# Performance work log

Hardware: AMD Instinct MI355X
Metric: run time of the kernel (lower is better)

Reference implementation:

```python
import jax, jax.numpy as jnp
import numpy as np

EPS = 1e-5
NEG_SLOPE = 0.2


def _batched_dynamic_conv(x, kernels):
    # x: [B, C, H, W]; kernels: [B, Cout, Cin, 3, 3]. Per-sample distinct
    # kernels == one grouped conv with feature_group_count = B.
    B, C, H, W = x.shape
    Cout = kernels.shape[1]
    xg = x.reshape(1, B * C, H, W)
    kg = kernels.reshape(B * Cout, C, 3, 3)
    y = jax.lax.conv_general_dilated(
        xg, kg, window_strides=(1, 1), padding=((1, 1), (1, 1)),
        feature_group_count=B,
        dimension_numbers=('NCHW', 'OIHW', 'NCHW'))
    return y.reshape(B, Cout, H, W)


def _instance_norm(y):
    # InstanceNorm2d(affine=False): per (b, c) over spatial dims, biased var.
    mean = jnp.mean(y, axis=(2, 3), keepdims=True)
    var = jnp.var(y, axis=(2, 3), keepdims=True)
    return (y - mean) * jax.lax.rsqrt(var + EPS)


def _leaky_relu(y):
    return jnp.where(y >= 0, y, NEG_SLOPE * y)


def setup_inputs() -> dict:
    key = jax.random.key(0)
    k1, k2, k3 = jax.random.split(key, 3)
    B, C, H, W = 16, 64, 128, 128
    x = jax.random.normal(k1, (B, C, H, W), dtype=jnp.float32)
    kernel1 = jax.random.normal(k2, (B, C, C, 3, 3), dtype=jnp.float32) * 0.05
    kernel2 = jax.random.normal(k3, (B, C, C, 3, 3), dtype=jnp.float32) * 0.05
    return {"x": x, "kernel1": kernel1, "kernel2": kernel2}


def reference(x, kernel1, kernel2):
    h = _leaky_relu(_instance_norm(_batched_dynamic_conv(x, kernel1)))
    h = _instance_norm(_batched_dynamic_conv(h, kernel2))
    return _leaky_relu(x + h)
```

## Files before the change

### kernel.cpp

```cpp
#include <hip/hip_runtime.h>
#include <stdint.h>
#include <stddef.h>

#define BATCH 16
#define CH    64
#define IH    128
#define IW    128
#define HW    (IH*IW)

#define PROW 8320
#define PB   1081600
#define SEG  2112

typedef __attribute__((ext_vector_type(8))) short short8;
typedef __attribute__((ext_vector_type(4))) short short4v;
typedef __attribute__((ext_vector_type(4))) float f32x4;
typedef __attribute__((ext_vector_type(2))) float f32x2;

__device__ __forceinline__ float bf2f(short s) {
    union { unsigned int u; float f; } v;
    v.u = ((unsigned int)(unsigned short)s) << 16;
    return v.f;
}
__device__ __forceinline__ short f2bf(float f) {
    union { float f; unsigned int u; } v; v.f = f;
    unsigned int r = v.u + 0x7fffu + ((v.u >> 16) & 1u);
    return (short)(r >> 16);
}

__device__ __forceinline__ void gload_lds16(const short* g, short* l) {
    __builtin_amdgcn_global_load_lds(
        (const __attribute__((address_space(1))) void*)g,
        (__attribute__((address_space(3))) void*)l, 16, 0, 0);
}

__global__ __launch_bounds__(256) void prep_all(const float* __restrict__ x,
                                                const float* __restrict__ w1,
                                                const float* __restrict__ w2,
                                                short* __restrict__ xpad,
                                                short* __restrict__ w1t,
                                                short* __restrict__ w2t) {
    const int bid = blockIdx.x;
    const int t = threadIdx.x;
    if (bid < 2048) {
        __shared__ float tile[CH * 129];
        const int b = bid >> 7;
        const int y = bid & 127;
        const float* src = x + (size_t)b * CH * HW + (size_t)y * IW;
        #pragma unroll
        for (int i = 0; i < 32; ++i) {
            int lin = i * 256 + t;
            int c = lin >> 7, xx = lin & 127;
            tile[c * 129 + xx] = src[(size_t)c * HW + xx];
        }
        __syncthreads();
        unsigned int* dst = (unsigned int*)(xpad) + (size_t)b * (PB / 2) + (size_t)(y + 1) * (PROW / 2);
        #pragma unroll
        for (int j = 0; j < 16; ++j) {
            int lin = j * 256 + t;
            int c2 = lin & 31, xx = lin >> 5;
            unsigned int lo = (unsigned int)(unsigned short)f2bf(tile[(2 * c2) * 129 + xx]);
            unsigned int hi = (unsigned int)(unsigned short)f2bf(tile[(2 * c2 + 1) * 129 + xx]);
            dst[(c2 >> 4) * 2080 + (xx + 1) * 16 + (c2 & 15)] = lo | (hi << 16);
        }
    } else if (bid < 2560) {
        int b2 = bid - 2048;
        const float* src = w1; short* dst = w1t;
        if (b2 >= 256) { src = w2; dst = w2t; b2 -= 256; }
        int gt = b2 * 256 + t;
        int ci   = gt & 31;
        int cout = (gt >> 5) & 63;
        int cc   = (gt >> 11) & 1;
        int b    = gt >> 12;
        const float* s = src + ((size_t)(b * 64 + cout)) * 576 + (cc * 32 + ci) * 9;
        short* d = dst + ((size_t)(b * 2 + cc) * 9) * 2048 + cout * 32 + ci;
        #pragma unroll
        for (int tap = 0; tap < 9; ++tap)
            d[tap * 2048] = f2bf(s[tap]);
    } else {
        int b2 = bid - 2560;
        short* p = xpad + (size_t)b2 * PB;
        const short8 z = {0,0,0,0,0,0,0,0};
        #pragma unroll
        for (int i = 0; i < 17; ++i) {
            int s = i * 256 + t;
            if (s >= 4128) break;
            if (s < 2080) {
                int row = (s < 1040) ? 0 : 129;
                int o = (s < 1040 ? s : s - 1040) * 8;
                *(short8*)&p[(size_t)row * PROW + o] = z;
            } else {
                int u = s - 2080;
                int k = u & 3, col = (u >> 2) & 1, cc = (u >> 3) & 1, pr = (u >> 4) + 1;
                *(short8*)&p[(size_t)pr * PROW + cc * 4160 + (col ? 129 * 32 : 0) + k * 8] = z;
            }
        }
    }
}

template<bool FUSED>
__global__ __launch_bounds__(256, 1) void conv_kernel(
    const short* __restrict__ in, const short* __restrict__ wt,
    short* __restrict__ out, const float* __restrict__ nrm,
    float* __restrict__ part_s, float* __restrict__ part_q) {

    __shared__ short act[2][12 * SEG];

    const int g    = blockIdx.x;
    const int b    = g >> 4;
    const int t    = threadIdx.x;
    const int lane = t & 63;
    const int wave = t >> 6;
    const int l15  = lane & 15;
    const int q    = lane >> 4;

    const short* inB = in + (size_t)b * PB;
    const short* wgl = wt + (size_t)b * 36864;
    const int aoff = l15 * 32 + q * 8;

    const int scc = wave & 1;
    f32x2 sb[8];
    if (FUSED) {
        const int ci0 = (lane & 3) * 8;
        #pragma unroll
        for (int j = 0; j < 8; ++j)
            sb[j] = ((const f32x2*)nrm)[b * CH + scc * 32 + ci0 + j];
    }

    short8 stg[15];


    auto stage_issue = [&](int tt, short* buf) {
        const int xp0 = (tt & 1) * 64;
        const int quad = ((g & 15) << 1) + (tt >> 1);
        #pragma unroll
        for (int k = 0; k < 3; ++k) {
            const int s = wave + k * 4;
            const int rg = quad * 4 + (s >> 1);
            const short* gseg = inB + (size_t)rg * PROW + (s & 1) * 4160 + xp0 * 32;
            short* lseg = buf + s * SEG;
            #pragma unroll
            for (int c = 0; c < 4; ++c)
                gload_lds16(gseg + c * 512 + lane * 8, lseg + c * 512);
            if (lane < 8)
                gload_lds16(gseg + 2048 + lane * 8, lseg + 2048);
        }
    };

    auto stage_load = [&](int tt) {
        const int xp0 = (tt & 1) * 64;
        const int quad = ((g & 15) << 1) + (tt >> 1);
        #pragma unroll
        for (int k = 0; k < 3; ++k) {
            const int s = wave + k * 4;
            const int rg = quad * 4 + (s >> 1);
            const short* gseg = inB + (size_t)rg * PROW + (s & 1) * 4160 + xp0 * 32;
            #pragma unroll
            for (int c = 0; c < 5; ++c) {
                short8 v = {0,0,0,0,0,0,0,0};
                if (c < 4 || lane < 8)
                    v = *(const short8*)&gseg[c * 512 + lane * 8];
                stg[k * 5 + c] = v;
            }
        }
    };

    auto stage_write = [&](int tt, short* buf) {
        const int ph2 = tt & 1;
        const int quad = ((g & 15) << 1) + (tt >> 1);
        #pragma unroll
        for (int k = 0; k < 3; ++k) {
            const int s = wave + k * 4;
            const int rg = quad * 4 + (s >> 1);
            const bool rowpad = (rg == 0) || (rg == 129);
            short* lseg = buf + s * SEG;
            #pragma unroll
            for (int c = 0; c < 5; ++c) {
                if (c < 4 || lane < 8) {
                    short8 v = stg[k * 5 + c];
                    const int lpx = c * 16 + (lane >> 2);
                    const bool xm = (ph2 == 0 && lpx == 0) || (ph2 == 1 && lpx == 65);
                    short8 o;
                    if (rowpad || xm) {
                        o = (short8){0,0,0,0,0,0,0,0};
                    } else {
                        #pragma unroll
                        for (int j = 0; j < 8; ++j) {
                            float f = sb[j].x * bf2f(v[j]) + sb[j].y;
                            f = f >= 0.f ? f : 0.2f * f;
                            o[j] = f2bf(f);
                        }
                    }
                    *(short8*)&lseg[c * 512 + lane * 8] = o;
                }
            }
        }
    };

    short8 a2[2][4];
    #pragma unroll
    for (int mi = 0; mi < 4; ++mi)
        a2[0][mi] = *(const short8*)&wgl[aoff + mi * 512];

    if (FUSED) { stage_load(0); stage_write(0, act[0]); }
    else       stage_issue(0, act[0]);
    __syncthreads();

    #pragma unroll 1
    for (int tt = 0; tt < 4; ++tt) {
        short* bufr = act[tt & 1];
        short* bufw = act[(tt + 1) & 1];

        if (tt < 3) {
            if (FUSED) stage_load(tt + 1);
            else       stage_issue(tt + 1, bufw);
        }

        const int ph2 = tt & 1;
        const int quad = ((g & 15) << 1) + (tt >> 1);
        const int xp0 = ph2 * 64;
        const int y0 = quad * 4 + wave;

        const f32x4 zero4 = {0.f, 0.f, 0.f, 0.f};
        f32x4 acc[4][4];
        #pragma unroll
        for (int mi = 0; mi < 4; ++mi)
            #pragma unroll
            for (int ni = 0; ni < 4; ++ni) acc[mi][ni] = zero4;

        #pragma unroll
        for (int s = 0; s < 18; ++s) {
            const int cc = s / 9, tap = s % 9;
            const int dy = tap / 3, dx = tap % 3;
            const short* anext = wgl + (((s + 1) % 18) * 2048) + aoff;
            #pragma unroll
            for (int mi = 0; mi < 4; ++mi)
                a2[(s + 1) & 1][mi] = *(const short8*)&anext[mi * 512];
            const int segb = ((wave + dy) * 2 + cc) * SEG;
            short8 bb[4];
            #pragma unroll
            for (int ni = 0; ni < 4; ++ni)
                bb[ni] = *(const short8*)&bufr[segb + (dx + ni * 16 + l15) * 32 + q * 8];
            #pragma unroll
            for (int mi = 0; mi < 4; ++mi)
                #pragma unroll
                for (int ni = 0; ni < 4; ++ni)
                    acc[mi][ni] = __builtin_amdgcn_mfma_f32_16x16x32_bf16(
                        a2[s & 1][mi], bb[ni], acc[mi][ni], 0, 0, 0);
        }

        if (FUSED && tt < 3) stage_write(tt + 1, bufw);

        const int pbase = ((b * 128 + y0) * 2 + ph2) * 64;
        #pragma unroll
        for (int mi = 0; mi < 4; ++mi) {
            float psum[4] = {0.f,0.f,0.f,0.f};
            float psq[4]  = {0.f,0.f,0.f,0.f};
            #pragma unroll
            for (int ni = 0; ni < 4; ++ni) {
                int xx = xp0 + ni * 16 + l15;
                size_t base = (size_t)b * PB + (size_t)(1 + y0) * PROW
                              + (mi >> 1) * 4160 + (size_t)(1 + xx) * 32
                              + (mi & 1) * 16 + q * 4;
                short4v o;
                #pragma unroll
                for (int gg = 0; gg < 4; ++gg) {
                    float v = acc[mi][ni][gg];
                    o[gg] = f2bf(v);
                    psum[gg] += v;
                    psq[gg]  += v * v;
                }
                *(short4v*)&out[base] = o;
            }
            #pragma unroll
            for (int gg = 0; gg < 4; ++gg) {
                float s = psum[gg], s2 = psq[gg];
                #pragma unroll
                for (int off = 1; off < 16; off <<= 1) {
                    s  += __shfl_xor(s,  off, 64);
                    s2 += __shfl_xor(s2, off, 64);
                }
                if (l15 == 0) {
                    int idx = pbase + mi * 16 + q * 4 + gg;
                    part_s[idx] = s;
                    part_q[idx] = s2;
                }
            }
        }

        __syncthreads();
    }
}

__global__ __launch_bounds__(256) void finalize_stats(const float* __restrict__ part_s,
                                                      const float* __restrict__ part_q,
                                                      float* __restrict__ nrm) {
    __shared__ float red[2][4][64];
    const int b = blockIdx.x;
    const int c = threadIdx.x & 63;
    const int g = threadIdx.x >> 6;
    const float* ps = part_s + (size_t)b * 16384 + c;
    const float* pq = part_q + (size_t)b * 16384 + c;
    float s = 0.f, s2 = 0.f;
    #pragma unroll 8
    for (int r = 0; r < 64; ++r) {
        s  += ps[(g * 64 + r) * 64];
        s2 += pq[(g * 64 + r) * 64];
    }
    red[0][g][c] = s;
    red[1][g][c] = s2;
    __syncthreads();
    if (threadIdx.x < 64) {
        float S = red[0][0][c] + red[0][1][c] + red[0][2][c] + red[0][3][c];
        float Q = red[1][0][c] + red[1][1][c] + red[1][2][c] + red[1][3][c];
        const float inv = 1.0f / (float)HW;
        float mean = S * inv;
        float var = Q * inv - mean * mean;
        float scale = rsqrtf(var + 1e-5f);
        f32x2 sb = {scale, -mean * scale};
        ((f32x2*)nrm)[b * CH + c] = sb;
    }
}

__global__ __launch_bounds__(256) void final_kernel(const float* __restrict__ x,
                                                    const short* __restrict__ y2,
                                                    const float* __restrict__ nrm,
                                                    float* __restrict__ out) {
    __shared__ float tile[64 * 65];
    const int x0 = blockIdx.x * 64;
    const int y  = blockIdx.y;
    const int b  = blockIdx.z;
    const int t  = threadIdx.x;
    const f32x2* nb = (const f32x2*)nrm + b * CH;
    const size_t rowb = (size_t)b * PB + (size_t)(y + 1) * PROW;
    #pragma unroll
    for (int i = 0; i < 2; ++i) {
        int s = i * 256 + t;
        int xx = s >> 3;
        int c0 = (s & 7) * 8;
        int cc = c0 >> 5, cl = c0 & 31;
        short8 v = *(const short8*)&y2[rowb + cc * 4160 + (size_t)(x0 + xx + 1) * 32 + cl];
        #pragma unroll
        for (int j = 0; j < 8; ++j) {
            f32x2 sb = nb[c0 + j];
            tile[(c0 + j) * 65 + xx] = sb.x * bf2f(v[j]) + sb.y;
        }
    }
    __syncthreads();
    #pragma unroll
    for (int i = 0; i < 4; ++i) {
        int lin = i * 1024 + t * 4;
        int c = lin >> 6;
        int xx = lin & 63;
        size_t g = ((size_t)(b * CH + c) * IH + y) * IW + x0 + xx;
        f32x4 xv = *(const f32x4*)&x[g];
        f32x4 o;
        #pragma unroll
        for (int k = 0; k < 4; ++k) {
            float f = xv[k] + tile[c * 65 + xx + k];
            o[k] = f >= 0.f ? f : 0.2f * f;
        }
        *(f32x4*)&out[g] = o;
    }
}

extern "C" void kernel_launch(void* const* d_in, const int* in_sizes, int n_in,
                              void* d_out, int out_size, void* d_ws, size_t ws_size,
                              hipStream_t stream) {
    const float* x  = (const float*)d_in[0];
    const float* w1 = (const float*)d_in[1];
    const float* w2 = (const float*)d_in[2];
    float* out = (float*)d_out;
    char* ws = (char*)d_ws;

    const size_t SZ_PAD  = 34611200ull;
    const size_t SZ_PART = 1048576ull;
    short* xpad = (short*)(ws);
    short* hpad = (short*)(ws + SZ_PAD);
    short* w1t  = (short*)(ws + 2 * SZ_PAD);
    short* w2t  = (short*)(ws + 2 * SZ_PAD + 1179648ull);
    float* ps1  = (float*)(ws + 2 * SZ_PAD + 2359296ull);
    float* pq1  = (float*)(ws + 2 * SZ_PAD + 2359296ull + SZ_PART);
    float* ps2  = (float*)(ws + 2 * SZ_PAD + 2359296ull + 2 * SZ_PART);
    float* pq2  = (float*)(ws + 2 * SZ_PAD + 2359296ull + 3 * SZ_PART);
    float* nrm1 = (float*)(ws + 2 * SZ_PAD + 2359296ull + 4 * SZ_PART);
    float* nrm2 = nrm1 + BATCH * CH * 2;

    if (ws_size < 2 * SZ_PAD + 2359296ull + 4 * SZ_PART + 8192) return;

    prep_all<<<2576, 256, 0, stream>>>(x, w1, w2, xpad, w1t, w2t);
    conv_kernel<false><<<256, 256, 0, stream>>>(xpad, w1t, hpad, nullptr, ps1, pq1);
    finalize_stats<<<16, 256, 0, stream>>>(ps1, pq1, nrm1);
    conv_kernel<true><<<256, 256, 0, stream>>>(hpad, w2t, xpad, nrm1, ps2, pq2);
    finalize_stats<<<16, 256, 0, stream>>>(ps2, pq2, nrm2);
    final_kernel<<<dim3(2, 128, 16), 256, 0, stream>>>(x, xpad, nrm2, out);
}
```

Measured before the change: 243.3 us.

## Split conv kernel into producer staging waves and MFMA consumer waves

```diff
diff --git a/kernel.cpp b/kernel.cpp
--- a/kernel.cpp
+++ b/kernel.cpp
@@ -99,7 +99,7 @@
 }
 
 template<bool FUSED>
-__global__ __launch_bounds__(256, 1) void conv_kernel(
+__global__ __launch_bounds__(512, 2) void conv_kernel(
     const short* __restrict__ in, const short* __restrict__ wt,
     short* __restrict__ out, const float* __restrict__ nrm,
     float* __restrict__ part_s, float* __restrict__ part_q) {
@@ -118,177 +118,173 @@
     const short* wgl = wt + (size_t)b * 36864;
     const int aoff = l15 * 32 + q * 8;
 
-    const int scc = wave & 1;
-    f32x2 sb[8];
-    if (FUSED) {
-        const int ci0 = (lane & 3) * 8;
-        #pragma unroll
-        for (int j = 0; j < 8; ++j)
-            sb[j] = ((const f32x2*)nrm)[b * CH + scc * 32 + ci0 + j];
-    }
-
-    short8 stg[15];
-
-
-    auto stage_issue = [&](int tt, short* buf) {
-        const int xp0 = (tt & 1) * 64;
-        const int quad = ((g & 15) << 1) + (tt >> 1);
-        #pragma unroll
-        for (int k = 0; k < 3; ++k) {
-            const int s = wave + k * 4;
-            const int rg = quad * 4 + (s >> 1);
-            const short* gseg = inB + (size_t)rg * PROW + (s & 1) * 4160 + xp0 * 32;
-            short* lseg = buf + s * SEG;
+    if (wave >= 4) {
+        const int p = wave - 4;
+        f32x2 sb[8];
+        if (FUSED) {
+            const int scc = p & 1;
+            const int ci0 = (lane & 3) * 8;
             #pragma unroll
-            for (int c = 0; c < 4; ++c)
-                gload_lds16(gseg + c * 512 + lane * 8, lseg + c * 512);
-            if (lane < 8)
-                gload_lds16(gseg + 2048 + lane * 8, lseg + 2048);
-        }
-    };
-
-    auto stage_load = [&](int tt) {
-        const int xp0 = (tt & 1) * 64;
-        const int quad = ((g & 15) << 1) + (tt >> 1);
-        #pragma unroll
-        for (int k = 0; k < 3; ++k) {
-            const int s = wave + k * 4;
-            const int rg = quad * 4 + (s >> 1);
-            const short* gseg = inB + (size_t)rg * PROW + (s & 1) * 4160 + xp0 * 32;
-            #pragma unroll
-            for (int c = 0; c < 5; ++c) {
-                short8 v = {0,0,0,0,0,0,0,0};
-                if (c < 4 || lane < 8)
-                    v = *(const short8*)&gseg[c * 512 + lane * 8];
-                stg[k * 5 + c] = v;
+            for (int j = 0; j < 8; ++j)
+                sb[j] = ((const f32x2*)nrm)[b * CH + scc * 32 + ci0 + j];
+        }
+
+        auto stage = [&](int tt, short* buf) {
+            const int ph2 = tt & 1;
+            const int xp0 = ph2 * 64;
+            const int quad = ((g & 15) << 1) + (tt >> 1);
+            if (!FUSED) {
+                #pragma unroll
+                for (int k = 0; k < 3; ++k) {
+                    const int s = p + k * 4;
+                    const int rg = quad * 4 + (s >> 1);
+                    const short* gseg = inB + (size_t)rg * PROW + (s & 1) * 4160 + xp0 * 32;
+                    short* lseg = buf + s * SEG;
+                    #pragma unroll
+                    for (int c = 0; c < 4; ++c)
+                        gload_lds16(gseg + c * 512 + lane * 8, lseg + c * 512);
+                    if (lane < 8)
+                        gload_lds16(gseg + 2048 + lane * 8, lseg + 2048);
+                }
+            } else {
+                short8 stg[15];
+                #pragma unroll
+                for (int k = 0; k < 3; ++k) {
+                    const int s = p + k * 4;
+                    const int rg = quad * 4 + (s >> 1);
+                    const short* gseg = inB + (size_t)rg * PROW + (s & 1) * 4160 + xp0 * 32;
+                    #pragma unroll
+                    for (int c = 0; c < 5; ++c) {
+                        short8 v = {0,0,0,0,0,0,0,0};
+                        if (c < 4 || lane < 8)
+                            v = *(const short8*)&gseg[c * 512 + lane * 8];
+                        stg[k * 5 + c] = v;
+                    }
+                }
+                #pragma unroll
+                for (int k = 0; k < 3; ++k) {
+                    const int s = p + k * 4;
+                    const int rg = quad * 4 + (s >> 1);
+                    const bool rowpad = (rg == 0) || (rg == 129);
+                    short* lseg = buf + s * SEG;
+                    #pragma unroll
+                    for (int c = 0; c < 5; ++c) {
+                        if (c < 4 || lane < 8) {
+                            short8 v = stg[k * 5 + c];
+                            const int lpx = c * 16 + (lane >> 2);
+                            const bool xm = (ph2 == 0 && lpx == 0) || (ph2 == 1 && lpx == 65);
+                            short8 o;
+                            if (rowpad || xm) {
+                                o = (short8){0,0,0,0,0,0,0,0};
+                            } else {
+                                #pragma unroll
+                                for (int j = 0; j < 8; ++j) {
+                                    float f = sb[j].x * bf2f(v[j]) + sb[j].y;
+                                    f = f >= 0.f ? f : 0.2f * f;
+                                    o[j] = f2bf(f);
+                                }
+                            }
+                            *(short8*)&lseg[c * 512 + lane * 8] = o;
+                        }
+                    }
+                }
             }
-        }
-    };
-
-    auto stage_write = [&](int tt, short* buf) {
-        const int ph2 = tt & 1;
-        const int quad = ((g & 15) << 1) + (tt >> 1);
-        #pragma unroll
-        for (int k = 0; k < 3; ++k) {
-            const int s = wave + k * 4;
-            const int rg = quad * 4 + (s >> 1);
-            const bool rowpad = (rg == 0) || (rg == 129);
-            short* lseg = buf + s * SEG;
-            #pragma unroll
-            for (int c = 0; c < 5; ++c) {
-                if (c < 4 || lane < 8) {
-                    short8 v = stg[k * 5 + c];
-                    const int lpx = c * 16 + (lane >> 2);
-                    const bool xm = (ph2 == 0 && lpx == 0) || (ph2 == 1 && lpx == 65);
-                    short8 o;
-                    if (rowpad || xm) {
-                        o = (short8){0,0,0,0,0,0,0,0};
-                    } else {
-                        #pragma unroll
-                        for (int j = 0; j < 8; ++j) {
-                            float f = sb[j].x * bf2f(v[j]) + sb[j].y;
-                            f = f >= 0.f ? f : 0.2f * f;
-                            o[j] = f2bf(f);
-                        }
-                    }
-                    *(short8*)&lseg[c * 512 + lane * 8] = o;
-                }
-            }
-        }
-    };
-
-    short8 a2[2][4];
-    #pragma unroll
-    for (int mi = 0; mi < 4; ++mi)
-        a2[0][mi] = *(const short8*)&wgl[aoff + mi * 512];
-
-    if (FUSED) { stage_load(0); stage_write(0, act[0]); }
-    else       stage_issue(0, act[0]);
-    __syncthreads();
-
-    #pragma unroll 1
-    for (int tt = 0; tt < 4; ++tt) {
-        short* bufr = act[tt & 1];
-        short* bufw = act[(tt + 1) & 1];
-
-        if (tt < 3) {
-            if (FUSED) stage_load(tt + 1);
-            else       stage_issue(tt + 1, bufw);
-        }
-
-        const int ph2 = tt & 1;
-        const int quad = ((g & 15) << 1) + (tt >> 1);
-        const int xp0 = ph2 * 64;
-        const int y0 = quad * 4 + wave;
-
-        const f32x4 zero4 = {0.f, 0.f, 0.f, 0.f};
-        f32x4 acc[4][4];
-        #pragma unroll
-        for (int mi = 0; mi < 4; ++mi)
-            #pragma unroll
-            for (int ni = 0; ni < 4; ++ni) acc[mi][ni] = zero4;
-
-        #pragma unroll
-        for (int s = 0; s < 18; ++s) {
-            const int cc = s / 9, tap = s % 9;
-            const int dy = tap / 3, dx = tap % 3;
-            const short* anext = wgl + (((s + 1) % 18) * 2048) + aoff;
+        };
+
+        stage(0, act[0]);
+        __syncthreads();
+        #pragma unroll 1
+        for (int tt = 0; tt < 4; ++tt) {
+            if (tt < 3) stage(tt + 1, act[(tt + 1) & 1]);
+            __syncthreads();
+        }
+    } else {
+        short8 a2[4][4];
+        #pragma unroll
+        for (int mi = 0; mi < 4; ++mi) {
+            a2[0][mi] = *(const short8*)&wgl[aoff + mi * 512];
+            a2[1][mi] = *(const short8*)&wgl[2048 + aoff + mi * 512];
+        }
+        __syncthreads();
+
+        #pragma unroll 1
+        for (int tt = 0; tt < 4; ++tt) {
+            const short* bufr = act[tt & 1];
+            const int ph2 = tt & 1;
+            const int quad = ((g & 15) << 1) + (tt >> 1);
+            const int xp0 = ph2 * 64;
+            const int y0 = quad * 4 + wave;
+
+            const f32x4 zero4 = {0.f, 0.f, 0.f, 0.f};
+            f32x4 acc[4][4];
             #pragma unroll
             for (int mi = 0; mi < 4; ++mi)
-                a2[(s + 1) & 1][mi] = *(const short8*)&anext[mi * 512];
-            const int segb = ((wave + dy) * 2 + cc) * SEG;
-            short8 bb[4];
+                #pragma unroll
+                for (int ni = 0; ni < 4; ++ni) acc[mi][ni] = zero4;
+
             #pragma unroll
-            for (int ni = 0; ni < 4; ++ni)
-                bb[ni] = *(const short8*)&bufr[segb + (dx + ni * 16 + l15) * 32 + q * 8];
+            for (int s = 0; s < 18; ++s) {
+                const int cc = s / 9, tap = s % 9;
+                const int dy = tap / 3, dx = tap % 3;
+                const int segb = ((wave + dy) * 2 + cc) * SEG;
+                short8 bb[4];
+                #pragma unroll
+                for (int ni = 0; ni < 4; ++ni)
+                    bb[ni] = *(const short8*)&bufr[segb + (dx + ni * 16 + l15) * 32 + q * 8];
+                #pragma unroll
+                for (int mi = 0; mi < 4; ++mi)
+                    #pragma unroll
+                    for (int ni = 0; ni < 4; ++ni)
+                        acc[mi][ni] = __builtin_amdgcn_mfma_f32_16x16x32_bf16(
+                            a2[s & 3][mi], bb[ni], acc[mi][ni], 0, 0, 0);
+                {
+                    const int nl = (s + 2) % 18;
+                    const short* anext = wgl + nl * 2048 + aoff;
+                    #pragma unroll
+                    for (int mi = 0; mi < 4; ++mi)
+                        a2[nl & 3][mi] = *(const short8*)&anext[mi * 512];
+                }
+            }
+
+            const int pbase = ((b * 128 + y0) * 2 + ph2) * 64;
             #pragma unroll
-            for (int mi = 0; mi < 4; ++mi)
-                #pragma unroll
-                for (int ni = 0; ni < 4; ++ni)
-                    acc[mi][ni] = __builtin_amdgcn_mfma_f32_16x16x32_bf16(
-                        a2[s & 1][mi], bb[ni], acc[mi][ni], 0, 0, 0);
-        }
-
-        if (FUSED && tt < 3) stage_write(tt + 1, bufw);
-
-        const int pbase = ((b * 128 + y0) * 2 + ph2) * 64;
-        #pragma unroll
-        for (int mi = 0; mi < 4; ++mi) {
-            float psum[4] = {0.f,0.f,0.f,0.f};
-            float psq[4]  = {0.f,0.f,0.f,0.f};
-            #pragma unroll
-            for (int ni = 0; ni < 4; ++ni) {
-                int xx = xp0 + ni * 16 + l15;
-                size_t base = (size_t)b * PB + (size_t)(1 + y0) * PROW
-                              + (mi >> 1) * 4160 + (size_t)(1 + xx) * 32
-                              + (mi & 1) * 16 + q * 4;
-                short4v o;
+            for (int mi = 0; mi < 4; ++mi) {
+                float psum[4] = {0.f,0.f,0.f,0.f};
+                float psq[4]  = {0.f,0.f,0.f,0.f};
+                #pragma unroll
+                for (int ni = 0; ni < 4; ++ni) {
+                    int xx = xp0 + ni * 16 + l15;
+                    size_t base = (size_t)b * PB + (size_t)(1 + y0) * PROW
+                                  + (mi >> 1) * 4160 + (size_t)(1 + xx) * 32
+                                  + (mi & 1) * 16 + q * 4;
+                    short4v o;
+                    #pragma unroll
+                    for (int gg = 0; gg < 4; ++gg) {
+                        float v = acc[mi][ni][gg];
+                        o[gg] = f2bf(v);
+                        psum[gg] += v;
+                        psq[gg]  += v * v;
+                    }
+                    *(short4v*)&out[base] = o;
+                }
                 #pragma unroll
                 for (int gg = 0; gg < 4; ++gg) {
-                    float v = acc[mi][ni][gg];
-                    o[gg] = f2bf(v);
-                    psum[gg] += v;
-                    psq[gg]  += v * v;
-                }
-                *(short4v*)&out[base] = o;
+                    float s = psum[gg], s2 = psq[gg];
+                    #pragma unroll
+                    for (int off = 1; off < 16; off <<= 1) {
+                        s  += __shfl_xor(s,  off, 64);
+                        s2 += __shfl_xor(s2, off, 64);
+                    }
+                    if (l15 == 0) {
+                        int idx = pbase + mi * 16 + q * 4 + gg;
+                        part_s[idx] = s;
+                        part_q[idx] = s2;
+                    }
+                }
             }
-            #pragma unroll
-            for (int gg = 0; gg < 4; ++gg) {
-                float s = psum[gg], s2 = psq[gg];
-                #pragma unroll
-                for (int off = 1; off < 16; off <<= 1) {
-                    s  += __shfl_xor(s,  off, 64);
-                    s2 += __shfl_xor(s2, off, 64);
-                }
-                if (l15 == 0) {
-                    int idx = pbase + mi * 16 + q * 4 + gg;
-                    part_s[idx] = s;
-                    part_q[idx] = s2;
-                }
-            }
-        }
-
-        __syncthreads();
+
+            __syncthreads();
+        }
     }
 }
 
@@ -389,9 +385,9 @@
     if (ws_size < 2 * SZ_PAD + 2359296ull + 4 * SZ_PART + 8192) return;
 
     prep_all<<<2576, 256, 0, stream>>>(x, w1, w2, xpad, w1t, w2t);
-    conv_kernel<false><<<256, 256, 0, stream>>>(xpad, w1t, hpad, nullptr, ps1, pq1);
+    conv_kernel<false><<<256, 512, 0, stream>>>(xpad, w1t, hpad, nullptr, ps1, pq1);
     finalize_stats<<<16, 256, 0, stream>>>(ps1, pq1, nrm1);
-    conv_kernel<true><<<256, 256, 0, stream>>>(hpad, w2t, xpad, nrm1, ps2, pq2);
+    conv_kernel<true><<<256, 512, 0, stream>>>(hpad, w2t, xpad, nrm1, ps2, pq2);
     finalize_stats<<<16, 256, 0, stream>>>(ps2, pq2, nrm2);
     final_kernel<<<dim3(2, 128, 16), 256, 0, stream>>>(x, xpad, nrm2, out);
 }
```

Measured after the change: 326.2 us. 1.34x slower.
